# Optimization experiments

Measured on AMD Instinct MI355X. Metric: run time of the kernel, lower is better.

Reference implementation:

```python
import jax, jax.numpy as jnp
import numpy as np

N_SAMPLES = 2 ** 15            # 32768
N_FRAMES = N_SAMPLES // 256    # 128 (window 512, step 256)
N_EVENTS = 8
N_HARM = 8
TOTAL_COEFFS = N_SAMPLES // 2 + 1
NOISE_SPEC = 16
NYQUIST = 22050.0 / 2.0
MAX_F = 3000.0 / NYQUIST
MIN_F = 20.0 / NYQUIST
F_SPAN = MAX_F - MIN_F
Y = 20 + NOISE_SPEC + N_FRAMES + N_HARM   # 172
DIM = Y + 128 + 128                        # 428
BATCH = 16


def lin_interp(x, out_size):
    # torch F.interpolate(mode='linear', align_corners=False) along last dim
    n = x.shape[-1]
    scale = n / out_size
    coords = jnp.clip((jnp.arange(out_size) + 0.5) * scale - 0.5, 0.0, n - 1.0)
    lo = jnp.floor(coords).astype(jnp.int32)
    hi = jnp.minimum(lo + 1, n - 1)
    w = (coords - lo).astype(x.dtype)
    return x[..., lo] * (1.0 - w) + x[..., hi] * w


def setup_inputs() -> dict:
    key = jax.random.key(0)
    k1, k2 = jax.random.split(key)
    x = jax.random.normal(k1, (BATCH, N_EVENTS, DIM), dtype=jnp.float32)
    noise = jax.random.uniform(k2, (BATCH, N_EVENTS, N_SAMPLES), dtype=jnp.float32)
    return {"x": x, "noise": noise}


def reference(x, noise):
    B = x.shape[0]
    x = jax.nn.sigmoid(x)
    means = x[..., 0:1]
    stds = x[..., 1:2] * 0.1
    amps = x[..., 2:3] ** 2
    f0 = x[..., 3:4] ** 2
    factors = 1.0 + x[..., 4:12] * 7.0
    mags = (x[..., 12:20] * 0.9999) ** 2
    noise_coeff = x[..., 20:20 + NOISE_SPEC]
    fine_env = x[..., 36:36 + N_FRAMES] * 2.0 - 1.0
    amp_factors = x[..., 164:172] ** 2
    f0_var = x[..., 172:300]

    # fine amplitude envelope: cumsum over frames, clamp, upsample
    fe = jnp.clip(jnp.cumsum(fine_env.reshape(-1, N_FRAMES), axis=-1), 0.0, 1.0)
    fe = lin_interp(fe, N_SAMPLES).reshape(B, N_EVENTS, N_SAMPLES)

    # localized band-limited noise, gaussian time window
    rng = jnp.arange(N_SAMPLES, dtype=x.dtype)
    mu = jnp.clip(means * N_SAMPLES, -(N_SAMPLES // 2), N_SAMPLES * 1.5)
    sigma = jnp.clip((1e-8 + stds) * N_SAMPLES, 0.0, N_SAMPLES - 1.0)
    z = (rng - mu) / sigma                                   # (B,E,S)
    probs = jnp.exp(-0.5 * z * z) / (sigma * np.sqrt(2.0 * np.pi))
    probs = probs / (jnp.max(jnp.abs(probs), axis=-1, keepdims=True) + 1e-12)
    u = noise * 2.0 - 1.0                                    # uniform(-1,1)
    spec_shape = lin_interp(noise_coeff, TOTAL_COEFFS)       # (B,E,total_coeffs)
    ns = jnp.fft.rfft(u, axis=-1, norm='ortho') * spec_shape
    nz = jnp.fft.irfft(ns, n=N_SAMPLES, axis=-1, norm='ortho')
    atoms = probs * nz * amps * fe                           # (B,E,S)

    # harmonic resonance
    f0f = f0.reshape(-1, 1)                                  # (BE,1)
    var = f0_var.reshape(-1, N_FRAMES) * (f0f * 0.01)        # (BE,F)
    f0t = lin_interp(f0f + var, N_SAMPLES)                   # (BE,S)
    f0t = MIN_F + f0t * F_SPAN
    f0t = jnp.where(f0t > 1.0, 0.0, f0t)
    fac = factors.reshape(-1, N_HARM).at[:, 0].set(1.0)      # (BE,H)
    freqs = f0t[:, None, :] * fac[:, :, None] * np.pi        # (BE,H,S)
    osc = jnp.sin(jnp.cumsum(freqs, axis=-1)) * amp_factors.reshape(-1, N_HARM, 1)
    # cumprod of a constant per frame == geometric powers
    mg = mags.reshape(-1, N_HARM, 1) ** jnp.arange(1, N_FRAMES + 1, dtype=x.dtype)
    mg = lin_interp(mg, N_SAMPLES)                           # (BE,H,S)
    res = jnp.sum(osc * mg, axis=1).reshape(B, N_EVENTS, N_SAMPLES)

    # fft convolution (zero-padded to 2S to avoid circular wrap)
    pa = jnp.pad(atoms, ((0, 0), (0, 0), (0, N_SAMPLES)))
    pr = jnp.pad(res, ((0, 0), (0, 0), (0, N_SAMPLES)))
    conv = jnp.fft.irfft(jnp.fft.rfft(pa, axis=-1) * jnp.fft.rfft(pr, axis=-1),
                         n=2 * N_SAMPLES, axis=-1)[..., :N_SAMPLES]
    return jnp.sum(conv, axis=1, keepdims=True)              # (B,1,S)
```

## Files before the change

### kernel.cpp

```cpp
#include <hip/hip_runtime.h>
#include <math.h>

#define NSAMP 32768
#define NFFT2 65536
#define NFRM 128
#define PSTRIDE 2688
#define P_FEPAIR 64
#define P_PW2 320
#define P_LQ 1344
#define P_AF 1604
#define P_END 2636
#define TWO_PI_F 6.28318530717958647692f

typedef float2 cplx;

__device__ __forceinline__ cplx cmul_(cplx a, cplx b){ return make_float2(a.x*b.x - a.y*b.y, a.x*b.y + a.y*b.x); }
__device__ __forceinline__ cplx cadd_(cplx a, cplx b){ return make_float2(a.x+b.x, a.y+b.y); }
__device__ __forceinline__ cplx csub_(cplx a, cplx b){ return make_float2(a.x-b.x, a.y-b.y); }

__device__ __forceinline__ unsigned int packbf2(float re, float im){
  unsigned int ur = __float_as_uint(re);
  unsigned int ui = __float_as_uint(im);
  ur = (ur + 0x7FFFu + ((ur>>16)&1u)) >> 16;
  ui = (ui + 0x7FFFu + ((ui>>16)&1u)) & 0xFFFF0000u;
  return ur | ui;
}
__device__ __forceinline__ float ubf_lo(unsigned int u){ return __uint_as_float(u<<16); }
__device__ __forceinline__ float ubf_hi(unsigned int u){ return __uint_as_float(u & 0xFFFF0000u); }
__device__ __forceinline__ unsigned short packbf1(float v){
  unsigned int u=__float_as_uint(v);
  return (unsigned short)((u + 0x7FFFu + ((u>>16)&1u))>>16);
}
__device__ __forceinline__ float unpackbf1(unsigned short s){ return __uint_as_float(((unsigned int)s)<<16); }

template<bool INV>
__device__ __forceinline__ void dft4_(cplx x0,cplx x1,cplx x2,cplx x3, cplx&y0,cplx&y1,cplx&y2,cplx&y3){
  cplx t0=cadd_(x0,x2), t1=csub_(x0,x2), t2=cadd_(x1,x3), t3=csub_(x1,x3);
  y0=cadd_(t0,t2); y2=csub_(t0,t2);
  cplx it3 = make_float2(-t3.y, t3.x);
  if (INV){ y1=cadd_(t1,it3); y3=csub_(t1,it3); }
  else    { y1=csub_(t1,it3); y3=cadd_(t1,it3); }
}

template<bool INV>
__device__ __forceinline__ void dft8ip_(cplx* v){
  cplx e0,e1,e2,e3,o0,o1,o2,o3;
  dft4_<INV>(v[0],v[2],v[4],v[6], e0,e1,e2,e3);
  dft4_<INV>(v[1],v[3],v[5],v[7], o0,o1,o2,o3);
  const float r = 0.70710678118654752440f;
  cplx w1 = INV ? make_float2(r, r)    : make_float2(r,-r);
  cplx w2 = INV ? make_float2(0.f,1.f) : make_float2(0.f,-1.f);
  cplx w3 = INV ? make_float2(-r,r)    : make_float2(-r,-r);
  cplx t1 = cmul_(o1,w1), t2 = cmul_(o2,w2), t3 = cmul_(o3,w3);
  v[0]=cadd_(e0,o0); v[4]=csub_(e0,o0);
  v[1]=cadd_(e1,t1); v[5]=csub_(e1,t1);
  v[2]=cadd_(e2,t2); v[6]=csub_(e2,t2);
  v[3]=cadd_(e3,t3); v[7]=csub_(e3,t3);
}

template<bool INV>
__device__ __forceinline__ void dft16ip_(cplx* v){
  cplx t0[4], t1[4], t2[4], t3[4];
  dft4_<INV>(v[0], v[4], v[8],  v[12], t0[0],t0[1],t0[2],t0[3]);
  dft4_<INV>(v[1], v[5], v[9],  v[13], t1[0],t1[1],t1[2],t1[3]);
  dft4_<INV>(v[2], v[6], v[10], v[14], t2[0],t2[1],t2[2],t2[3]);
  dft4_<INV>(v[3], v[7], v[11], v[15], t3[0],t3[1],t3[2],t3[3]);
  const float C1=0.92387953251128675613f, S1=0.38268343236508977172f, R2=0.70710678118654752440f;
  #define TWD_(x, cc, ss) (INV ? cmul_((x), make_float2((cc), (ss))) : cmul_((x), make_float2((cc), -(ss))))
  t1[1] = TWD_(t1[1], C1, S1);
  t1[2] = TWD_(t1[2], R2, R2);
  t1[3] = TWD_(t1[3], S1, C1);
  t2[1] = TWD_(t2[1], R2, R2);
  t2[2] = TWD_(t2[2], 0.f, 1.f);
  t2[3] = TWD_(t2[3], -R2, R2);
  t3[1] = TWD_(t3[1], S1, C1);
  t3[2] = TWD_(t3[2], -R2, R2);
  t3[3] = TWD_(t3[3], -C1, -S1);
  #undef TWD_
  dft4_<INV>(t0[0], t1[0], t2[0], t3[0], v[0], v[4], v[8],  v[12]);
  dft4_<INV>(t0[1], t1[1], t2[1], t3[1], v[1], v[5], v[9],  v[13]);
  dft4_<INV>(t0[2], t1[2], t2[2], t3[2], v[2], v[6], v[10], v[14]);
  dft4_<INV>(t0[3], t1[3], t2[3], t3[3], v[3], v[7], v[11], v[15]);
}

template<int R0, bool INV>
__device__ __forceinline__ void fft_core(float* lre, float* lim, int t){
  constexpr int Q = R0/16;
  constexpr int S1 = R0 + 8;
  int g = t >> 4, a = t & 15;
  cplx v[Q];
  #pragma unroll
  for (int bb=0;bb<Q;bb++){ int idx = g*S1 + a + 16*bb; v[bb]=make_float2(lre[idx],lim[idx]); }
  if constexpr (Q==16) dft16ip_<INV>(v); else dft8ip_<INV>(v);
  float th = (INV?TWO_PI_F:-TWO_PI_F)*(float)a/(float)R0;
  float sn,cs; __sincosf(th,&sn,&cs);
  cplx w1=make_float2(cs,sn), wu=w1;
  #pragma unroll
  for (int c=1;c<Q;c++){ v[c]=cmul_(v[c],wu); wu=cmul_(wu,w1); }
  __syncthreads();
  #pragma unroll
  for (int c=0;c<Q;c++){ int m = a*Q + ((c+a)&(Q-1)); lre[g*S1+m]=v[c].x; lim[g*S1+m]=v[c].y; }
  __syncthreads();
}

template<int R0, bool INV>
__device__ __forceinline__ bool fft_stage2(const float* lre, const float* lim, int t, int& g2, int& c2, cplx* z){
  constexpr int Q = R0/16; constexpr int S1 = R0+8;
  bool active = (R0==256) || (t < 16*Q);
  g2 = (R0==256)?(t>>4):(t>>3);
  c2 = (R0==256)?(t&15):(t&7);
  if (active){
    #pragma unroll
    for (int a2=0;a2<16;a2++){ int m = a2*Q + ((c2+a2)&(Q-1)); z[a2]=make_float2(lre[g2*S1+m], lim[g2*S1+m]); }
    dft16ip_<INV>(z);
  }
  return active;
}

__global__ __launch_bounds__(256) void k_fft_pack_fwd1(const float* __restrict__ noise, unsigned int* __restrict__ dst, float interBase){
  constexpr int Q=16, S1=264;
  __shared__ float lre[4352], lim[4352];
  int t=threadIdx.x;
  int bx=blockIdx.x;
  int sig = bx>>3;
  int tBase=(bx&7)*16;
  const float* n0 = noise + (size_t)(2*sig)*NSAMP;
  const float* n1 = noise + (size_t)(2*sig+1)*NSAMP;
  #pragma unroll
  for (int i=0;i<16;i++){
    int e=t+256*i, g=e&15, r=e>>4;
    int ts = tBase+g+128*r;
    lre[g*S1+r]=n0[ts]*2.f-1.f;
    lim[g*S1+r]=n1[ts]*2.f-1.f;
  }
  __syncthreads();
  fft_core<256,false>(lre,lim,t);
  int g2,c2; cplx z[16];
  fft_stage2<256,false>(lre,lim,t,g2,c2,z);
  int p=tBase+g2;
  float thp=interBase*(float)p;
  float snc,csc; __sincosf(thp*(float)c2,&snc,&csc);
  float sns,css; __sincosf(thp*(float)Q,&sns,&css);
  cplx wu=make_float2(csc,snc), ws=make_float2(css,sns);
  unsigned int* db = dst + (size_t)sig*NSAMP;
  size_t ob=(size_t)256*(size_t)p+(size_t)c2;
  #pragma unroll
  for (int d=0;d<16;d++){
    cplx val = cmul_(z[d],wu);
    db[ob+(size_t)(d*16)] = packbf2(val.x, val.y);
    wu=cmul_(wu,ws);
  }
}

__device__ __forceinline__ void fft128_natural(float* re, float* im, int t){
  __syncthreads();
  fft_core<128,false>(re,im,t);
  int g2,c2; cplx z[16];
  bool act = fft_stage2<128,false>(re,im,t,g2,c2,z);
  __syncthreads();
  if (act){
    #pragma unroll
    for (int d=0;d<16;d++){ int u=c2+8*d; re[u*17+g2]=z[d].x; im[u*17+g2]=z[d].y; }
  }
  __syncthreads();
}

__global__ __launch_bounds__(256) void k_nfilter_ip1(const unsigned int* __restrict__ src, cplx* __restrict__ dst,
    const float* __restrict__ P){
  __shared__ float aRe[2176], aIm[2176], bRe[2176], bIm[2176];
  __shared__ float fRe[2176], fIm[2176];
  __shared__ float c1s[16], c2sh[16];
  int t=threadIdx.x, pb=blockIdx.x, j=blockIdx.y;
  const unsigned int* sb = src + ((size_t)j<<15);
  cplx* db = dst + ((size_t)j<<15);
  if (t<16) c1s[t] = P[(size_t)(2*j)*PSTRIDE+28+t];
  else if (t<32) c2sh[t-16] = P[(size_t)(2*j+1)*PSTRIDE+28+(t-16)];
  #pragma unroll
  for (int i=0;i<8;i++){
    int e=t+256*i, g=e&15, r=e>>4;
    int col = (pb<8)? (pb*16+g) : (g*16);
    unsigned int u = sb[col + (r<<8)];
    aRe[g*136+r]=ubf_lo(u); aIm[g*136+r]=ubf_hi(u);
  }
  fft128_natural(aRe,aIm,t);
  if (pb<8){
    #pragma unroll
    for (int i=0;i<8;i++){
      int e=t+256*i, g=e&15, r=e>>4;
      int col = 240-pb*16+g;
      unsigned int u = sb[col + (r<<8)];
      bRe[g*136+r]=ubf_lo(u); bIm[g*136+r]=ubf_hi(u);
    }
    fft128_natural(bRe,bIm,t);
  }
  const float inv32768 = 1.0f/32768.0f;
  if (pb<8){
    for (int s=0;s<2;s++){
      __syncthreads();
      #pragma unroll
      for (int uu=0; uu<8; uu++){
        int g=t&15, u=(t>>4)+16*uu;
        if (g!=0){
          int colK = s? (240-pb*16+g) : (pb*16+g);
          int gm=16-g, um=127-u;
          float Zkx,Zky,Zmx,Zmy;
          if (s==0){ Zkx=aRe[u*17+g]; Zky=aIm[u*17+g]; Zmx=bRe[um*17+gm]; Zmy=bIm[um*17+gm]; }
          else     { Zkx=bRe[u*17+g]; Zky=bIm[u*17+g]; Zmx=aRe[um*17+gm]; Zmy=aIm[um*17+gm]; }
          int k = colK + (u<<8);
          int kb = min(k, NSAMP-k);
          float coords=fminf(fmaxf((kb+0.5f)*(16.0f/16385.0f)-0.5f,0.0f),15.0f);
          int lo=(int)coords; float w=coords-lo; int hi=min(lo+1,15);
          float s1=(c1s[lo]+w*(c1s[hi]-c1s[lo]))*inv32768;
          float s2=(c2sh[lo]+w*(c2sh[hi]-c2sh[lo]))*inv32768;
          float U1x=0.5f*(Zkx+Zmx), U1y=0.5f*(Zky-Zmy);
          float U2x=0.5f*(Zky+Zmy), U2y=-0.5f*(Zkx-Zmx);
          fRe[g*136+u]=U1x*s1 - U2y*s2; fIm[g*136+u]=U1y*s1 + U2x*s2;
        }
      }
      __syncthreads();
      fft_core<128,true>(fRe,fIm,t);
      int gg,cc; cplx z[16];
      bool act = fft_stage2<128,true>(fRe,fIm,t,gg,cc,z);
      if (act && gg!=0){
        int p = (s==0) ? (pb*16+gg) : (240-pb*16+gg);
        float thp=(TWO_PI_F/32768.0f)*(float)p;
        float snc,csc; __sincosf(thp*(float)cc,&snc,&csc);
        float sns,css; __sincosf(thp*8.0f,&sns,&css);
        cplx wu=make_float2(csc,snc), wsx=make_float2(css,sns);
        int ob=128*p+cc;
        #pragma unroll
        for (int d=0;d<16;d++){ db[ob+8*d]=cmul_(z[d],wu); wu=cmul_(wu,wsx); }
      }
    }
  } else {
    __syncthreads();
    #pragma unroll
    for (int uu=0; uu<8; uu++){
      int g=t&15, u=(t>>4)+16*uu;
      int k = g*16 + (u<<8);
      int gm=(16-g)&15;
      int um=(g==0)? ((128-u)&127) : (127-u);
      float Zkx=aRe[u*17+g], Zky=aIm[u*17+g];
      float Zmx=aRe[um*17+gm], Zmy=aIm[um*17+gm];
      int kb = min(k, NSAMP-k);
      float coords=fminf(fmaxf((kb+0.5f)*(16.0f/16385.0f)-0.5f,0.0f),15.0f);
      int lo=(int)coords; float w=coords-lo; int hi=min(lo+1,15);
      float s1=(c1s[lo]+w*(c1s[hi]-c1s[lo]))*inv32768;
      float s2=(c2sh[lo]+w*(c2sh[hi]-c2sh[lo]))*inv32768;
      float U1x=0.5f*(Zkx+Zmx), U1y=0.5f*(Zky-Zmy);
      float U2x=0.5f*(Zky+Zmy), U2y=-0.5f*(Zkx-Zmx);
      fRe[g*136+u]=U1x*s1 - U2y*s2; fIm[g*136+u]=U1y*s1 + U2x*s2;
    }
    __syncthreads();
    fft_core<128,true>(fRe,fIm,t);
    int gg,cc; cplx z[16];
    bool act = fft_stage2<128,true>(fRe,fIm,t,gg,cc,z);
    if (act){
      int p = 16*gg;
      float thp=(TWO_PI_F/32768.0f)*(float)p;
      float snc,csc; __sincosf(thp*(float)cc,&snc,&csc);
      float sns,css; __sincosf(thp*8.0f,&sns,&css);
      cplx wu=make_float2(csc,snc), wsx=make_float2(css,sns);
      int ob=128*p+cc;
      #pragma unroll
      for (int d=0;d<16;d++){ db[ob+8*d]=cmul_(z[d],wu); wu=cmul_(wu,wsx); }
    }
  }
}

__global__ __launch_bounds__(256) void k_ifinal_split(const cplx* __restrict__ src, unsigned short* __restrict__ dsth){
  constexpr int S1=264;
  __shared__ float lre[4352], lim[4352];
  int t=threadIdx.x; int bx=blockIdx.x;
  int sig=bx>>3; int tBase=(bx&7)*16;
  const cplx* sb = src + (size_t)sig*NSAMP;
  #pragma unroll
  for (int i=0;i<16;i++){
    int e=t+256*i, g=e&15, r=e>>4;
    cplx vv = sb[tBase+g + (size_t)r*128];
    lre[g*S1+r]=vv.x; lim[g*S1+r]=vv.y;
  }
  __syncthreads();
  fft_core<256,true>(lre,lim,t);
  int g2,c2; cplx z[16];
  fft_stage2<256,true>(lre,lim,t,g2,c2,z);
  __syncthreads();
  #pragma unroll
  for (int d=0;d<16;d++){ int u=c2+16*d; lre[u*17+g2]=z[d].x; lim[u*17+g2]=z[d].y; }
  __syncthreads();
  unsigned short* p0 = dsth + (size_t)(2*sig)*NSAMP;
  unsigned short* p1 = dsth + (size_t)(2*sig+1)*NSAMP;
  #pragma unroll
  for (int i=0;i<16;i++){
    int e=t+256*i, g3=e&15, u=e>>4;
    int ts = tBase+g3+u*128;
    p0[ts]=packbf1(lre[u*17+g3]); p1[ts]=packbf1(lim[u*17+g3]);
  }
}

__global__ __launch_bounds__(256) void k_conv_build_fwd1(const float* __restrict__ P,
    const unsigned short* __restrict__ NZh, unsigned int* __restrict__ dst, int rowBase, float interBase){
  constexpr int Q=16, S1=264;
  __shared__ float smem[8448];
  float* lre = smem;
  float* lim = smem + 4224;
  float* sTab = smem;
  int t=threadIdx.x;
  int row = rowBase + blockIdx.y;
  int tBase = blockIdx.x*16;
  const float* Pr = P + (size_t)row*PSTRIDE;
  for (int i=t; i<P_END; i+=256) sTab[i] = Pr[i];
  __syncthreads();
  float mu=sTab[0], sigma=sTab[1], amp=sTab[2], pscale=sTab[3];
  float fac[8], mh[8];
  #pragma unroll
  for (int h=0;h<8;h++){ fac[h]=sTab[4+h]; mh[h]=sTab[12+h]; }
  const float2* fe2 = (const float2*)&sTab[P_FEPAIR];
  const float*  pw2 = &sTab[P_PW2];
  const float2* LQt = (const float2*)&sTab[P_LQ];
  const float*  Af  = &sTab[P_AF];
  const unsigned short* nzrow = NZh + (size_t)row*NSAMP;
  float vre[8], vim[8];
  #pragma unroll
  for (int i=0;i<8;i++){
    int e=t+256*i, g=e&15, r=e>>4;
    int ts = tBase + g + (r<<8);
    float cc=fminf(fmaxf((ts+0.5f)*(1.0f/256.0f)-0.5f,0.0f),127.0f);
    int lo=(int)cc; float w=cc-lo;
    float2 fp = fe2[lo];
    float fev = fp.x + w*fp.y;
    int slot, n0;
    if (ts<128){ slot=0; n0=ts+1; } else { int km=(ts-128)>>8; slot=km+1; n0=ts-127-(km<<8); }
    float nf=(float)n0, nf2=nf*nf;
    float2 lq = LQt[slot];
    float base = nf*lq.x + nf2*lq.y;
    float wm = (lo<127)? w : 0.0f;
    float resv=0.f;
    #pragma unroll
    for (int h=0;h<8;h++){
      float mgb = pw2[h*128+lo];
      if (mgb > 1e-7f){
        float rr = Af[slot*8+h] + fac[h]*base;
        float fr = rr - floorf(rr);
        float s = __builtin_amdgcn_sinf(fr);
        resv += s*mgb*(1.0f + wm*(mh[h]-1.0f));
      }
    }
    float zz=((float)ts-mu)/sigma;
    float prb=pscale*__expf(-0.5f*zz*zz);
    vre[i] = prb*unpackbf1(nzrow[ts])*amp*fev;
    vim[i] = resv;
  }
  __syncthreads();
  #pragma unroll
  for (int i=0;i<8;i++){
    int e=t+256*i, g=e&15, r=e>>4;
    lre[g*S1+r]=vre[i]; lim[g*S1+r]=vim[i];
  }
  #pragma unroll
  for (int i=8;i<16;i++){
    int e=t+256*i, g=e&15, r=e>>4;
    lre[g*S1+r]=0.f; lim[g*S1+r]=0.f;
  }
  __syncthreads();
  fft_core<256,false>(lre,lim,t);
  int g2,c2; cplx z[16];
  fft_stage2<256,false>(lre,lim,t,g2,c2,z);
  int p = tBase+g2;
  float thp = interBase*(float)p;
  float snc,csc; __sincosf(thp*(float)c2,&snc,&csc);
  float sns,css; __sincosf(thp*(float)Q,&sns,&css);
  cplx wu=make_float2(csc,snc), ws=make_float2(css,sns);
  unsigned int* db = dst + (size_t)blockIdx.y*NFFT2;
  size_t ob=(size_t)256*(size_t)p+(size_t)c2;
  #pragma unroll
  for (int d=0; d<16; d++){
    cplx val = cmul_(z[d],wu);
    db[ob+(size_t)(d*16)] = packbf2(val.x, val.y);
    wu=cmul_(wu,ws);
  }
}

__global__ __launch_bounds__(256) void k_sq_inv1(const unsigned int* __restrict__ C,
    unsigned int* __restrict__ E, int bpc){
  constexpr int Q=16, S1=264;
  __shared__ float lre[4352], lim[4352];
  int t=threadIdx.x;
  int tBase = blockIdx.x*16;
  int bLoc = blockIdx.y;
  int half = blockIdx.z;
  float accx[16], accy[16];
  #pragma unroll
  for (int d=0;d<16;d++){ accx[d]=0.f; accy[d]=0.f; }
  int g2=t>>4, c2=t&15;
  for (int e=0;e<4;e++){
    int sigLoc = bLoc*8 + half*4 + e;
    const unsigned int* sb = C + (size_t)sigLoc*NFFT2;
    __syncthreads();
    #pragma unroll
    for (int i=0;i<16;i++){
      int ee=t+256*i, g=ee&15, r=ee>>4;
      unsigned int u = sb[tBase+g + (size_t)r*256];
      lre[g*S1+r]=ubf_lo(u);
      lim[g*S1+r]=ubf_hi(u);
    }
    __syncthreads();
    fft_core<256,false>(lre,lim,t);
    int gg,cc; cplx z[16];
    fft_stage2<256,false>(lre,lim,t,gg,cc,z);
    #pragma unroll
    for (int d=0;d<16;d++){
      float x=z[d].x, y=z[d].y;
      accx[d] += x*x - y*y;
      accy[d] += 2.f*x*y;
    }
  }
  __syncthreads();
  const float s = 1.0f/131072.0f;
  #pragma unroll
  for (int d=0;d<16;d++){
    int rrow = c2 + 16*d;
    lre[g2*S1+rrow] = accx[d]*s;
    lim[g2*S1+rrow] = accy[d]*s;
  }
  __syncthreads();
  fft_core<256,true>(lre,lim,t);
  int gg,cc; cplx z[16];
  fft_stage2<256,true>(lre,lim,t,gg,cc,z);
  int p = tBase+gg;
  float thp = (TWO_PI_F/65536.0f)*(float)p;
  float snc,csc; __sincosf(thp*(float)cc,&snc,&csc);
  float sns,css; __sincosf(thp*(float)Q,&sns,&css);
  cplx wu=make_float2(csc,snc), ws=make_float2(css,sns);
  unsigned int* db = E + ((size_t)half*bpc + bLoc)*NFFT2;
  size_t ob=(size_t)256*(size_t)p+(size_t)cc;
  #pragma unroll
  for (int d=0; d<16; d++){
    cplx val = cmul_(z[d],wu);
    db[ob+(size_t)(d*16)] = packbf2(val.x, val.y);
    wu=cmul_(wu,ws);
  }
}

__global__ __launch_bounds__(256) void k_final_imout(const unsigned int* __restrict__ E,
    float* __restrict__ out, int batchBase, int bpc){
  constexpr int S1=264;
  __shared__ float lre[4352], lim[4352];
  int t=threadIdx.x; int bx=blockIdx.x;
  int sig=bx>>4; int tBase=(bx&15)*16;
  const unsigned int* s0 = E + (size_t)sig*NFFT2;
  size_t hstride = (size_t)bpc*NFFT2;
  #pragma unroll
  for (int i=0;i<16;i++){
    int e=t+256*i, g=e&15, r=e>>4;
    size_t idx = tBase+g+(size_t)r*256;
    unsigned int u0=s0[idx], u1=s0[hstride+idx];
    lre[g*S1+r]=ubf_lo(u0)+ubf_lo(u1);
    lim[g*S1+r]=ubf_hi(u0)+ubf_hi(u1);
  }
  __syncthreads();
  fft_core<256,true>(lre,lim,t);
  int g2,c2; cplx z[16];
  fft_stage2<256,true>(lre,lim,t,g2,c2,z);
  __syncthreads();
  #pragma unroll
  for (int d=0;d<16;d++){ int u=c2+16*d; lre[u*17+g2]=z[d].y; }
  __syncthreads();
  float* o = out + (size_t)(batchBase+sig)*NSAMP;
  #pragma unroll
  for (int i=0;i<8;i++){
    int e=t+256*i, g3=e&15, u=e>>4;
    o[tBase+g3 + u*256] = lre[u*17+g3];
  }
}

__global__ __launch_bounds__(256) void k_params(const float* __restrict__ x, float* __restrict__ P){
  int row = blockIdx.x; int t = threadIdx.x;
  const float* xr = x + row*428;
  float* Pr = P + (size_t)row*PSTRIDE;
  __shared__ float sx[428];
  __shared__ float fes[128], f0s[128];
  __shared__ double Cds[128];
  __shared__ float facs[8], ms[8], afs[8];
  __shared__ float f0_sh;
  for (int i=t;i<428;i+=256) sx[i]=1.0f/(1.0f+expf(-xr[i]));
  __syncthreads();
  if (t==0){
    float mean = sx[0]; float stds = sx[1]*0.1f; float amp = sx[2]*sx[2];
    float mu = fminf(fmaxf(mean*32768.0f, -16384.0f), 49152.0f);
    float sigma = fminf(fmaxf((1e-8f + stds)*32768.0f, 0.0f), 32767.0f);
    float c = 1.0f/(sigma*2.5066282746310002f);
    float tt0 = fminf(fmaxf(floorf(mu), 0.0f), 32767.0f);
    float tt1 = fminf(fmaxf(ceilf(mu), 0.0f), 32767.0f);
    float z0 = (tt0-mu)/sigma, z1=(tt1-mu)/sigma;
    float gmax = fmaxf(expf(-0.5f*z0*z0), expf(-0.5f*z1*z1));
    float pscale = c / (c*gmax + 1e-12f);
    Pr[0]=mu; Pr[1]=sigma; Pr[2]=amp; Pr[3]=pscale;
  }
  if (t<8){
    float fv = (t==0)?1.0f:(1.0f+sx[4+t]*7.0f);
    facs[t]=fv; Pr[4+t]=fv;
    float m = sx[12+t]*0.9999f; m=m*m; ms[t]=m; Pr[12+t]=m;
    afs[t]=sx[164+t]*sx[164+t];
  }
  if (t>=32&&t<48) Pr[28+(t-32)] = sx[20+(t-32)];
  if (t==64) f0_sh = sx[3]*sx[3];
  if (t==65){
    float acc=0.f;
    for (int f=0;f<128;f++){ acc += sx[36+f]*2.0f-1.0f; fes[f]=fminf(fmaxf(acc,0.f),1.f); }
  }
  __syncthreads();
  if (t<128){
    float f0=f0_sh;
    f0s[t] = f0 + sx[172+t]*(f0*0.01f);
  }
  __syncthreads();
  if (t==0){
    double acc = 128.0*(double)f0s[0]; Cds[0]=acc;
    for (int k=0;k<127;k++){ acc += 128.0*((double)f0s[k]+(double)f0s[k+1]); Cds[k+1]=acc; }
  }
  if (t<128){
    float v=fes[t], vh=fes[min(t+1,127)];
    Pr[P_FEPAIR+2*t]=v; Pr[P_FEPAIR+2*t+1]=vh-v;
  }
  if (t>=128 && t<136){
    int h=t-128; float m=ms[h];
    float acc = afs[h]*m;
    float* dstp = Pr + P_PW2 + h*128;
    dstp[0]=acc;
    for (int f=1;f<128;f++){ acc*=m; dstp[f]=acc; }
  }
  __syncthreads();
  const double MINF_D=20.0/11025.0, FSPAN_D=2980.0/11025.0;
  if (t<129){
    int k=t-1;
    float Lb, Qb;
    if (k<0){ Lb=(float)(0.5*(MINF_D+FSPAN_D*(double)f0s[0])); Qb=0.f; }
    else {
      double f0k=(double)f0s[k];
      double d=(k<127)?((double)f0s[k+1]-f0k):0.0;
      Lb=(float)(0.5*(MINF_D+FSPAN_D*f0k));
      Qb=(float)(0.5*FSPAN_D*d*(1.0/512.0));
    }
    Pr[P_LQ+2*t]=Lb; Pr[P_LQ+2*t+1]=Qb;
  }
  for (int idx=t; idx<129*8; idx+=256){
    int jj=idx>>3, h=idx&7, k=jj-1;
    float Aval;
    if (k<0) Aval=0.f;
    else {
      double phi0=(double)(128+256*k)*MINF_D+FSPAN_D*Cds[k];
      Aval=(float)(0.5*fmod((double)facs[h]*phi0,2.0));
    }
    Pr[P_AF+idx]=Aval;
  }
}

extern "C" void kernel_launch(void* const* d_in, const int* in_sizes, int n_in,
                              void* d_out, int out_size, void* d_ws, size_t ws_size,
                              hipStream_t stream){
  const float* x = (const float*)d_in[0];
  const float* noise = (const float*)d_in[1];
  float* out = (float*)d_out;
  char* ws = (char*)d_ws;

  const size_t szA = (size_t)64*NSAMP*sizeof(unsigned int);
  const size_t szB = (size_t)64*NSAMP*sizeof(cplx);
  const size_t szE = (size_t)2*16*NFFT2*sizeof(unsigned int);
  const size_t oA  = (size_t)2<<20;
  const size_t oB  = oA + szA;
  const size_t oE  = oB + szB;
  const size_t oC  = oE + szE;

  const int cand[5] = {1,2,4,8,16};
  int nchunk = -1;
  for (int ci=0; ci<5; ci++){
    size_t csz = ((size_t)(128/cand[ci]))*NFFT2*sizeof(unsigned int);
    if (oC + csz <= ws_size){ nchunk = cand[ci]; break; }
  }
  if (nchunk < 0) return;
  int sigPerChunk = 128/nchunk;
  int bpc = sigPerChunk/8;

  float* P = (float*)(ws);
  unsigned int* A = (unsigned int*)(ws + oA);
  cplx* B = (cplx*)(ws + oB);
  unsigned int* E = (unsigned int*)(ws + oE);
  unsigned int* C = (unsigned int*)(ws + oC);

  k_params<<<128, 256, 0, stream>>>(x, P);
  k_fft_pack_fwd1<<<512, 256, 0, stream>>>(noise, A, -TWO_PI_F/32768.0f);
  k_nfilter_ip1<<<dim3(9,64), 256, 0, stream>>>(A, B, P);
  k_ifinal_split<<<512, 256, 0, stream>>>(B, (unsigned short*)A);

  for (int c=0; c<nchunk; c++){
    int rowBase = c*sigPerChunk;
    int batchBase = c*bpc;
    k_conv_build_fwd1<<<dim3(16, sigPerChunk), 256, 0, stream>>>(P, (unsigned short*)A, C, rowBase, -TWO_PI_F/65536.0f);
    k_sq_inv1<<<dim3(16, bpc, 2), 256, 0, stream>>>(C, E, bpc);
    k_final_imout<<<bpc*16, 256, 0, stream>>>(E, out, batchBase, bpc);
  }
}
```

Before: 113.4 us.

## Fuse noise inverse FFT final pass into conv build kernel via shared-memory handoff

Removes the separate k_ifinal_split kernel and performs its final inverse-FFT pass inside the convolution build kernel. The filtered noise is kept in shared memory as packed bf16 pairs and consumed directly by the two rows of each signal. This drops one launch and the global round trip of the bf16 noise signal. In exchange, the grid has half as many blocks, each doing more serial work, and shared memory use per block grows, which may reduce occupancy and parallelism.

```diff
diff --git a/kernel.cpp b/kernel.cpp
--- a/kernel.cpp
+++ b/kernel.cpp
@@ -27,11 +27,6 @@
 }
 __device__ __forceinline__ float ubf_lo(unsigned int u){ return __uint_as_float(u<<16); }
 __device__ __forceinline__ float ubf_hi(unsigned int u){ return __uint_as_float(u & 0xFFFF0000u); }
-__device__ __forceinline__ unsigned short packbf1(float v){
-  unsigned int u=__float_as_uint(v);
-  return (unsigned short)((u + 0x7FFFu + ((u>>16)&1u))>>16);
-}
-__device__ __forceinline__ float unpackbf1(unsigned short s){ return __uint_as_float(((unsigned int)s)<<16); }
 
 template<bool INV>
 __device__ __forceinline__ void dft4_(cplx x0,cplx x1,cplx x2,cplx x3, cplx&y0,cplx&y1,cplx&y2,cplx&y3){
@@ -268,116 +263,118 @@
   }
 }
 
-__global__ __launch_bounds__(256) void k_ifinal_split(const cplx* __restrict__ src, unsigned short* __restrict__ dsth){
-  constexpr int S1=264;
-  __shared__ float lre[4352], lim[4352];
-  int t=threadIdx.x; int bx=blockIdx.x;
-  int sig=bx>>3; int tBase=(bx&7)*16;
-  const cplx* sb = src + (size_t)sig*NSAMP;
-  #pragma unroll
-  for (int i=0;i<16;i++){
-    int e=t+256*i, g=e&15, r=e>>4;
-    cplx vv = sb[tBase+g + (size_t)r*128];
-    lre[g*S1+r]=vv.x; lim[g*S1+r]=vv.y;
-  }
-  __syncthreads();
-  fft_core<256,true>(lre,lim,t);
-  int g2,c2; cplx z[16];
-  fft_stage2<256,true>(lre,lim,t,g2,c2,z);
-  __syncthreads();
-  #pragma unroll
-  for (int d=0;d<16;d++){ int u=c2+16*d; lre[u*17+g2]=z[d].x; lim[u*17+g2]=z[d].y; }
-  __syncthreads();
-  unsigned short* p0 = dsth + (size_t)(2*sig)*NSAMP;
-  unsigned short* p1 = dsth + (size_t)(2*sig+1)*NSAMP;
-  #pragma unroll
-  for (int i=0;i<16;i++){
-    int e=t+256*i, g3=e&15, u=e>>4;
-    int ts = tBase+g3+u*128;
-    p0[ts]=packbf1(lre[u*17+g3]); p1[ts]=packbf1(lim[u*17+g3]);
-  }
-}
-
-__global__ __launch_bounds__(256) void k_conv_build_fwd1(const float* __restrict__ P,
-    const unsigned short* __restrict__ NZh, unsigned int* __restrict__ dst, int rowBase, float interBase){
+__global__ __launch_bounds__(256) void k_iconv_build(const cplx* __restrict__ B,
+    const float* __restrict__ P, unsigned int* __restrict__ Cout, int sigBase, float interBase){
   constexpr int Q=16, S1=264;
   __shared__ float smem[8448];
+  __shared__ unsigned int nzl[4352];
   float* lre = smem;
   float* lim = smem + 4224;
   float* sTab = smem;
   int t=threadIdx.x;
-  int row = rowBase + blockIdx.y;
   int tBase = blockIdx.x*16;
-  const float* Pr = P + (size_t)row*PSTRIDE;
-  for (int i=t; i<P_END; i+=256) sTab[i] = Pr[i];
-  __syncthreads();
-  float mu=sTab[0], sigma=sTab[1], amp=sTab[2], pscale=sTab[3];
-  float fac[8], mh[8];
-  #pragma unroll
-  for (int h=0;h<8;h++){ fac[h]=sTab[4+h]; mh[h]=sTab[12+h]; }
-  const float2* fe2 = (const float2*)&sTab[P_FEPAIR];
-  const float*  pw2 = &sTab[P_PW2];
-  const float2* LQt = (const float2*)&sTab[P_LQ];
-  const float*  Af  = &sTab[P_AF];
-  const unsigned short* nzrow = NZh + (size_t)row*NSAMP;
-  float vre[8], vim[8];
-  #pragma unroll
-  for (int i=0;i<8;i++){
-    int e=t+256*i, g=e&15, r=e>>4;
-    int ts = tBase + g + (r<<8);
-    float cc=fminf(fmaxf((ts+0.5f)*(1.0f/256.0f)-0.5f,0.0f),127.0f);
-    int lo=(int)cc; float w=cc-lo;
-    float2 fp = fe2[lo];
-    float fev = fp.x + w*fp.y;
-    int slot, n0;
-    if (ts<128){ slot=0; n0=ts+1; } else { int km=(ts-128)>>8; slot=km+1; n0=ts-127-(km<<8); }
-    float nf=(float)n0, nf2=nf*nf;
-    float2 lq = LQt[slot];
-    float base = nf*lq.x + nf2*lq.y;
-    float wm = (lo<127)? w : 0.0f;
-    float resv=0.f;
-    #pragma unroll
-    for (int h=0;h<8;h++){
-      float mgb = pw2[h*128+lo];
-      if (mgb > 1e-7f){
-        float rr = Af[slot*8+h] + fac[h]*base;
-        float fr = rr - floorf(rr);
-        float s = __builtin_amdgcn_sinf(fr);
-        resv += s*mgb*(1.0f + wm*(mh[h]-1.0f));
+  int sig = sigBase + blockIdx.y;
+  {
+    const cplx* sb = B + (size_t)sig*NSAMP;
+    #pragma unroll
+    for (int i=0;i<16;i++){
+      int e=t+256*i, g=e&15, r=e>>4;
+      cplx vv = sb[tBase+g + (size_t)r*128];
+      lre[g*S1+r]=vv.x; lim[g*S1+r]=vv.y;
+    }
+    __syncthreads();
+    fft_core<256,true>(lre,lim,t);
+    int g2,c2; cplx z[16];
+    fft_stage2<256,true>(lre,lim,t,g2,c2,z);
+    #pragma unroll
+    for (int d=0;d<16;d++){
+      int u = c2 + 16*d;
+      nzl[u*17+g2] = packbf2(z[d].x, z[d].y);
+    }
+  }
+  for (int rr=0; rr<2; rr++){
+    int row = 2*sig + rr;
+    int rowLocal = row - 2*sigBase;
+    const float* Pr = P + (size_t)row*PSTRIDE;
+    __syncthreads();
+    for (int i=t; i<P_END; i+=256) sTab[i] = Pr[i];
+    __syncthreads();
+    float mu=sTab[0], sigma=sTab[1], amp=sTab[2], pscale=sTab[3];
+    float fac[8], mh[8];
+    #pragma unroll
+    for (int h=0;h<8;h++){ fac[h]=sTab[4+h]; mh[h]=sTab[12+h]; }
+    const float2* fe2 = (const float2*)&sTab[P_FEPAIR];
+    const float*  pw2 = &sTab[P_PW2];
+    const float2* LQt = (const float2*)&sTab[P_LQ];
+    const float*  Af  = &sTab[P_AF];
+    float vre[2][8], vim[2][8];
+    #pragma unroll
+    for (int inst=0; inst<2; inst++){
+      int tB = tBase + inst*128;
+      #pragma unroll
+      for (int i=0;i<8;i++){
+        int e=t+256*i, g=e&15, r=e>>4;
+        int ts = tB + g + (r<<8);
+        float cc=fminf(fmaxf((ts+0.5f)*(1.0f/256.0f)-0.5f,0.0f),127.0f);
+        int lo=(int)cc; float w=cc-lo;
+        float2 fp = fe2[lo];
+        float fev = fp.x + w*fp.y;
+        int slot, n0;
+        if (ts<128){ slot=0; n0=ts+1; } else { int km=(ts-128)>>8; slot=km+1; n0=ts-127-(km<<8); }
+        float nf=(float)n0, nf2=nf*nf;
+        float2 lq = LQt[slot];
+        float base = nf*lq.x + nf2*lq.y;
+        float wm = (lo<127)? w : 0.0f;
+        float resv=0.f;
+        #pragma unroll
+        for (int h=0;h<8;h++){
+          float mgb = pw2[h*128+lo];
+          if (mgb > 1e-7f){
+            float rv = Af[slot*8+h] + fac[h]*base;
+            float fr = rv - floorf(rv);
+            resv += __builtin_amdgcn_sinf(fr)*mgb*(1.0f + wm*(mh[h]-1.0f));
+          }
+        }
+        float zz=((float)ts-mu)/sigma;
+        float prb=pscale*__expf(-0.5f*zz*zz);
+        unsigned int unz = nzl[(inst + 2*r)*17 + g];
+        float nzv = rr ? ubf_hi(unz) : ubf_lo(unz);
+        vre[inst][i] = prb*nzv*amp*fev;
+        vim[inst][i] = resv;
       }
     }
-    float zz=((float)ts-mu)/sigma;
-    float prb=pscale*__expf(-0.5f*zz*zz);
-    vre[i] = prb*unpackbf1(nzrow[ts])*amp*fev;
-    vim[i] = resv;
-  }
-  __syncthreads();
-  #pragma unroll
-  for (int i=0;i<8;i++){
-    int e=t+256*i, g=e&15, r=e>>4;
-    lre[g*S1+r]=vre[i]; lim[g*S1+r]=vim[i];
-  }
-  #pragma unroll
-  for (int i=8;i<16;i++){
-    int e=t+256*i, g=e&15, r=e>>4;
-    lre[g*S1+r]=0.f; lim[g*S1+r]=0.f;
-  }
-  __syncthreads();
-  fft_core<256,false>(lre,lim,t);
-  int g2,c2; cplx z[16];
-  fft_stage2<256,false>(lre,lim,t,g2,c2,z);
-  int p = tBase+g2;
-  float thp = interBase*(float)p;
-  float snc,csc; __sincosf(thp*(float)c2,&snc,&csc);
-  float sns,css; __sincosf(thp*(float)Q,&sns,&css);
-  cplx wu=make_float2(csc,snc), ws=make_float2(css,sns);
-  unsigned int* db = dst + (size_t)blockIdx.y*NFFT2;
-  size_t ob=(size_t)256*(size_t)p+(size_t)c2;
-  #pragma unroll
-  for (int d=0; d<16; d++){
-    cplx val = cmul_(z[d],wu);
-    db[ob+(size_t)(d*16)] = packbf2(val.x, val.y);
-    wu=cmul_(wu,ws);
+    #pragma unroll
+    for (int inst=0; inst<2; inst++){
+      __syncthreads();
+      int tB = tBase + inst*128;
+      #pragma unroll
+      for (int i=0;i<8;i++){
+        int e=t+256*i, g=e&15, r=e>>4;
+        lre[g*S1+r]=vre[inst][i]; lim[g*S1+r]=vim[inst][i];
+      }
+      #pragma unroll
+      for (int i=8;i<16;i++){
+        int e=t+256*i, g=e&15, r=e>>4;
+        lre[g*S1+r]=0.f; lim[g*S1+r]=0.f;
+      }
+      __syncthreads();
+      fft_core<256,false>(lre,lim,t);
+      int g2,c2; cplx z[16];
+      fft_stage2<256,false>(lre,lim,t,g2,c2,z);
+      int p = tB+g2;
+      float thp = interBase*(float)p;
+      float snc,csc; __sincosf(thp*(float)c2,&snc,&csc);
+      float sns,css; __sincosf(thp*(float)Q,&sns,&css);
+      cplx wu=make_float2(csc,snc), ws=make_float2(css,sns);
+      unsigned int* db = Cout + (size_t)rowLocal*NFFT2;
+      size_t ob=(size_t)256*(size_t)p+(size_t)c2;
+      #pragma unroll
+      for (int d=0; d<16; d++){
+        cplx val = cmul_(z[d],wu);
+        db[ob+(size_t)(d*16)] = packbf2(val.x, val.y);
+        wu=cmul_(wu,ws);
+      }
+    }
   }
 }
 
@@ -581,6 +578,7 @@
   if (nchunk < 0) return;
   int sigPerChunk = 128/nchunk;
   int bpc = sigPerChunk/8;
+  int nsigs = sigPerChunk/2;
 
   float* P = (float*)(ws);
   unsigned int* A = (unsigned int*)(ws + oA);
@@ -591,12 +589,11 @@
   k_params<<<128, 256, 0, stream>>>(x, P);
   k_fft_pack_fwd1<<<512, 256, 0, stream>>>(noise, A, -TWO_PI_F/32768.0f);
   k_nfilter_ip1<<<dim3(9,64), 256, 0, stream>>>(A, B, P);
-  k_ifinal_split<<<512, 256, 0, stream>>>(B, (unsigned short*)A);
 
   for (int c=0; c<nchunk; c++){
-    int rowBase = c*sigPerChunk;
+    int sigBase = c*nsigs;
     int batchBase = c*bpc;
-    k_conv_build_fwd1<<<dim3(16, sigPerChunk), 256, 0, stream>>>(P, (unsigned short*)A, C, rowBase, -TWO_PI_F/65536.0f);
+    k_iconv_build<<<dim3(8, nsigs), 256, 0, stream>>>(B, P, C, sigBase, -TWO_PI_F/65536.0f);
     k_sq_inv1<<<dim3(16, bpc, 2), 256, 0, stream>>>(C, E, bpc);
     k_final_imout<<<bpc*16, 256, 0, stream>>>(E, out, batchBase, bpc);
   }
```

New measurement: 143.0 us. 1.26x slower.
